# Kernel tuning notes

Measured on AMD Instinct MI355X. Metric: run time of the kernel, lower is better.

Reference implementation:

```python
import jax, jax.numpy as jnp
import numpy as np

B, L, D = 32, 2048, 1024


def setup_inputs() -> dict:
    key = jax.random.key(0)
    ks = jax.random.split(key, 8)
    s = 1.0 / np.sqrt(D).astype(np.float32)  # torch nn.Linear init scale
    return {
        "decoder_hidden": jax.random.normal(ks[0], (B, 1, D), jnp.float32),
        "encoder_outputs": jax.random.normal(ks[1], (B, L, D), jnp.float32),
        "W_w": jax.random.uniform(ks[2], (D, D), jnp.float32, -s, s),
        "W_b": jax.random.uniform(ks[3], (D,), jnp.float32, -s, s),
        "U_w": jax.random.uniform(ks[4], (D, D), jnp.float32, -s, s),
        "U_b": jax.random.uniform(ks[5], (D,), jnp.float32, -s, s),
        "v_w": jax.random.uniform(ks[6], (1, D), jnp.float32, -s, s),
        "v_b": jax.random.uniform(ks[7], (1,), jnp.float32, -s, s),
    }


def reference(decoder_hidden, encoder_outputs, W_w, W_b, U_w, U_b, v_w, v_b):
    # torch Linear: y = x @ W.T + b
    q = decoder_hidden @ W_w.T + W_b            # [B, 1, D]
    k = encoder_outputs @ U_w.T + U_b           # [B, L, D]
    scores = jnp.tanh(q + k) @ v_w.T + v_b      # [B, L, 1]
    attn = jax.nn.softmax(scores[..., 0], axis=-1)[:, None, :]  # [B, 1, L]
    context = jnp.einsum("bql,bld->bqd", attn, encoder_outputs)  # [B, 1, D]
    return (context, attn)
```

## Files before the change

kernel.cpp:

```cpp
#include <hip/hip_runtime.h>
#include <hip/hip_bf16.h>
#include <stdint.h>

#define BB 32
#define LL 2048
#define DD 1024

typedef short short8  __attribute__((ext_vector_type(8)));
typedef float f32x4   __attribute__((ext_vector_type(4)));

__device__ __forceinline__ short f2bf(float f) {
    unsigned u = __float_as_uint(f);
    u += 0x7fffu + ((u >> 16) & 1u);
    return (short)(u >> 16);
}

__device__ __forceinline__ float bf2f(unsigned short s) {
    return __uint_as_float(((unsigned)s) << 16);
}

__device__ __forceinline__ float fast_tanh(float x) {
    float e = __expf(2.f * x);
    return 1.f - 2.f * __builtin_amdgcn_rcpf(e + 1.f);
}

__device__ __forceinline__ void async_cp16(const void* g, void* l) {
    __builtin_amdgcn_global_load_lds(
        (__attribute__((address_space(1))) void*)g,
        (__attribute__((address_space(3))) void*)l, 16, 0, 0);
}

__global__ void cvt_bf16_kernel(const float* __restrict__ src, short* __restrict__ dst) {
    int idx = (blockIdx.x * 256 + threadIdx.x) * 8;
    float4 a = *(const float4*)(src + idx);
    float4 c = *(const float4*)(src + idx + 4);
    short8 p;
    p[0] = f2bf(a.x); p[1] = f2bf(a.y); p[2] = f2bf(a.z); p[3] = f2bf(a.w);
    p[4] = f2bf(c.x); p[5] = f2bf(c.y); p[6] = f2bf(c.z); p[7] = f2bf(c.w);
    *(short8*)(dst + idx) = p;
}

__global__ void q_kernel(const float* __restrict__ dh, const float* __restrict__ Ww,
                         const float* __restrict__ Wb, const float* __restrict__ Ub,
                         float* __restrict__ qbuf) {
    int b  = blockIdx.x >> 4;
    int d0 = (blockIdx.x & 15) << 6;
    int t = threadIdx.x, w = t >> 6, lane = t & 63;
    __shared__ __align__(16) float hs[DD];
    *(float4*)&hs[t * 4] = *(const float4*)&dh[b * DD + t * 4];
    __syncthreads();
    float hr[16];
#pragma unroll
    for (int i = 0; i < 16; i++) hr[i] = hs[lane + 64 * i];
    for (int i = 0; i < 16; i++) {
        int d = d0 + w * 16 + i;
        const float* wr = Ww + (size_t)d * DD;
        float s = 0.f;
#pragma unroll
        for (int j = 0; j < 16; j++) s += wr[lane + 64 * j] * hr[j];
#pragma unroll
        for (int m = 1; m < 64; m <<= 1) s += __shfl_xor(s, m, 64);
        if (lane == 0) qbuf[b * DD + d] = s + Wb[d] + Ub[d];
    }
}

__global__ __launch_bounds__(256, 3) void gemm_scores_bf(
    const short* __restrict__ encbf, const short* __restrict__ Ubf,
    const float* __restrict__ qbuf, const float* __restrict__ vw,
    float* __restrict__ spart) {
    __shared__ __align__(16) short As[128 * 32];
    __shared__ __align__(16) short Bs[128 * 32];
    __shared__ float q_s[128], v_s[128], s_acc[2][128];

    const int t = threadIdx.x;
    const int lane = t & 63, w = t >> 6;
    const int l15 = lane & 15, quad = lane >> 4;
    const int wm = w >> 1, wn = w & 1;

    const int lin  = blockIdx.x + (blockIdx.y << 3);
    const int xcd  = lin & 7;
    const int slot = lin >> 3;
    const int nblk = slot & 7;
    const int mstripe = (xcd << 6) + (slot >> 3);
    const int n0 = nblk << 7;
    const int m0 = mstripe << 7;
    const int b  = m0 >> 11;

    if (t < 128) {
        q_s[t] = qbuf[(b << 10) + n0 + t];
        v_s[t] = vw[n0 + t];
    }

    f32x4 acc[4][4];
#pragma unroll
    for (int i = 0; i < 4; i++)
#pragma unroll
        for (int j = 0; j < 4; j++) acc[i][j] = (f32x4){0.f, 0.f, 0.f, 0.f};

    const int srow = lane >> 2, sseg = (lane & 3) << 3;
    const short* gA0 = encbf + (((size_t)(m0 + w * 32 + srow)) << 10) + sseg;
    const short* gB0 = Ubf   + (((size_t)(n0 + w * 32 + srow)) << 10) + sseg;
    short* lA0 = As + w * 32 * 32;
    short* lB0 = Bs + w * 32 * 32;

    for (int k0 = 0; k0 < 1024; k0 += 32) {
        __syncthreads();
        async_cp16(gA0 + k0, lA0);
        async_cp16(gA0 + k0 + (16 << 10), lA0 + 16 * 32);
        async_cp16(gB0 + k0, lB0);
        async_cp16(gB0 + k0 + (16 << 10), lB0 + 16 * 32);
        __syncthreads();

        short8 af[4], bfv[4];
#pragma unroll
        for (int mt = 0; mt < 4; mt++)
            af[mt] = *(const short8*)&As[(wm * 64 + mt * 16 + l15) * 32 + quad * 8];
#pragma unroll
        for (int nt = 0; nt < 4; nt++)
            bfv[nt] = *(const short8*)&Bs[(wn * 64 + nt * 16 + l15) * 32 + quad * 8];
#pragma unroll
        for (int mt = 0; mt < 4; mt++)
#pragma unroll
            for (int nt = 0; nt < 4; nt++)
                acc[mt][nt] = __builtin_amdgcn_mfma_f32_16x16x32_bf16(
                    af[mt], bfv[nt], acc[mt][nt], 0, 0, 0);
    }

    float qn[4], vn[4];
#pragma unroll
    for (int nt = 0; nt < 4; nt++) {
        qn[nt] = q_s[wn * 64 + nt * 16 + l15];
        vn[nt] = v_s[wn * 64 + nt * 16 + l15];
    }
#pragma unroll
    for (int mt = 0; mt < 4; mt++) {
#pragma unroll
        for (int r = 0; r < 4; r++) {
            float sum = 0.f;
#pragma unroll
            for (int nt = 0; nt < 4; nt++)
                sum += vn[nt] * fast_tanh(acc[mt][nt][r] + qn[nt]);
            sum += __shfl_xor(sum, 1, 64);
            sum += __shfl_xor(sum, 2, 64);
            sum += __shfl_xor(sum, 4, 64);
            sum += __shfl_xor(sum, 8, 64);
            if (l15 == 0)
                s_acc[wn][wm * 64 + mt * 16 + quad * 4 + r] = sum;
        }
    }
    __syncthreads();
    if (t < 128)
        spart[((size_t)nblk << 16) + m0 + t] = s_acc[0][t] + s_acc[1][t];
}

__global__ void ctx_softmax_bf(const float* __restrict__ sp, const short* __restrict__ encbf,
                               float* __restrict__ attn, float* __restrict__ ctx) {
    const int dchunk = blockIdx.x, b = blockIdx.y;
    const int t = threadIdx.x;
    const int w = t >> 6, lane = t & 63;
    __shared__ float at_s[2048];
    __shared__ float red[16][128];
    __shared__ float rr[8];

    float v[4];
#pragma unroll
    for (int i = 0; i < 4; i++) {
        int l = t + (i << 9);
        float s = 0.f;
#pragma unroll
        for (int p = 0; p < 8; p++) s += sp[(p << 16) + (b << 11) + l];
        v[i] = s;
    }
    float m = fmaxf(fmaxf(v[0], v[1]), fmaxf(v[2], v[3]));
#pragma unroll
    for (int s = 1; s < 64; s <<= 1) m = fmaxf(m, __shfl_xor(m, s, 64));
    if (lane == 0) rr[w] = m;
    __syncthreads();
    m = rr[0];
#pragma unroll
    for (int i = 1; i < 8; i++) m = fmaxf(m, rr[i]);
    float s = 0.f;
#pragma unroll
    for (int i = 0; i < 4; i++) { v[i] = __expf(v[i] - m); s += v[i]; }
#pragma unroll
    for (int k = 1; k < 64; k <<= 1) s += __shfl_xor(s, k, 64);
    __syncthreads();
    if (lane == 0) rr[w] = s;
#pragma unroll
    for (int i = 0; i < 4; i++) at_s[t + (i << 9)] = v[i];
    __syncthreads();
    s = 0.f;
#pragma unroll
    for (int i = 0; i < 8; i++) s += rr[i];
    float inv = 1.f / s;

    if (dchunk == 0) {
#pragma unroll
        for (int i = 0; i < 4; i++) attn[(b << 11) + t + (i << 9)] = v[i] * inv;
    }

    const int d4 = (t & 31) << 2;
    const int dl = t >> 5;
    const int d0 = dchunk << 7;
    const short* base = encbf + ((size_t)b << 21) + d0 + d4;
    float ax = 0.f, ay = 0.f, az = 0.f, aw = 0.f;
#pragma unroll 4
    for (int i = 0; i < 128; i++) {
        int l = (i << 4) + dl;
        float wg = at_s[l];
        ushort4 e = *(const ushort4*)(base + ((size_t)l << 10));
        ax += wg * bf2f(e.x); ay += wg * bf2f(e.y);
        az += wg * bf2f(e.z); aw += wg * bf2f(e.w);
    }
    red[dl][d4 + 0] = ax;
    red[dl][d4 + 1] = ay;
    red[dl][d4 + 2] = az;
    red[dl][d4 + 3] = aw;
    __syncthreads();
    if (t < 128) {
        float acc = 0.f;
#pragma unroll
        for (int j = 0; j < 16; j++) acc += red[j][t];
        ctx[(b << 10) + d0 + t] = acc * inv;
    }
}

__global__ __launch_bounds__(256, 3) void gemm_scores_f32(
    const float* __restrict__ enc, const short* __restrict__ Ubf,
    const float* __restrict__ qbuf, const float* __restrict__ vw,
    float* __restrict__ scores) {
    __shared__ __align__(16) short As[128 * 32];
    __shared__ __align__(16) short Bs[128 * 32];
    __shared__ float q_s[128], v_s[128], s_acc[128];

    const int t = threadIdx.x;
    const int lane = t & 63, w = t >> 6;
    const int l15 = lane & 15, quad = lane >> 4;
    const int wm = w >> 1, wn = w & 1;
    const int n0 = blockIdx.x << 7;
    const int m0 = blockIdx.y << 7;
    const int b  = m0 >> 11;

    if (t < 128) {
        q_s[t] = qbuf[(b << 10) + n0 + t];
        v_s[t] = vw[n0 + t];
        s_acc[t] = 0.f;
    }

    f32x4 acc[4][4];
#pragma unroll
    for (int i = 0; i < 4; i++)
#pragma unroll
        for (int j = 0; j < 4; j++) acc[i][j] = (f32x4){0.f, 0.f, 0.f, 0.f};

    const int arow = t >> 1, ahalf = t & 1;
    const float* aptr = enc + (((size_t)(m0 + arow)) << 10) + (ahalf << 4);
    short* adst = As + arow * 32 + ahalf * 16;
    const int brow = t >> 2, bks = (t & 3) * 8;
    const short* bptr1 = Ubf + ((size_t)(n0 + brow)) * 1024 + bks;
    const short* bptr2 = bptr1 + (size_t)64 * 1024;
    short* bdst1 = Bs + brow * 32 + bks;
    short* bdst2 = bdst1 + 64 * 32;

    for (int k0 = 0; k0 < 1024; k0 += 32) {
        __syncthreads();
        float4 f0 = *(const float4*)(aptr + k0);
        float4 f1 = *(const float4*)(aptr + k0 + 4);
        float4 f2 = *(const float4*)(aptr + k0 + 8);
        float4 f3 = *(const float4*)(aptr + k0 + 12);
        short8 p0, p1;
        p0[0] = f2bf(f0.x); p0[1] = f2bf(f0.y); p0[2] = f2bf(f0.z); p0[3] = f2bf(f0.w);
        p0[4] = f2bf(f1.x); p0[5] = f2bf(f1.y); p0[6] = f2bf(f1.z); p0[7] = f2bf(f1.w);
        p1[0] = f2bf(f2.x); p1[1] = f2bf(f2.y); p1[2] = f2bf(f2.z); p1[3] = f2bf(f2.w);
        p1[4] = f2bf(f3.x); p1[5] = f2bf(f3.y); p1[6] = f2bf(f3.z); p1[7] = f2bf(f3.w);
        *(short8*)adst = p0;
        *(short8*)(adst + 8) = p1;
        *(short8*)bdst1 = *(const short8*)(bptr1 + k0);
        *(short8*)bdst2 = *(const short8*)(bptr2 + k0);
        __syncthreads();

        short8 af[4], bfv[4];
#pragma unroll
        for (int mt = 0; mt < 4; mt++)
            af[mt] = *(const short8*)&As[(wm * 64 + mt * 16 + l15) * 32 + quad * 8];
#pragma unroll
        for (int nt = 0; nt < 4; nt++)
            bfv[nt] = *(const short8*)&Bs[(wn * 64 + nt * 16 + l15) * 32 + quad * 8];
#pragma unroll
        for (int mt = 0; mt < 4; mt++)
#pragma unroll
            for (int nt = 0; nt < 4; nt++)
                acc[mt][nt] = __builtin_amdgcn_mfma_f32_16x16x32_bf16(
                    af[mt], bfv[nt], acc[mt][nt], 0, 0, 0);
    }

    float qn[4], vn[4];
#pragma unroll
    for (int nt = 0; nt < 4; nt++) {
        qn[nt] = q_s[wn * 64 + nt * 16 + l15];
        vn[nt] = v_s[wn * 64 + nt * 16 + l15];
    }
#pragma unroll
    for (int mt = 0; mt < 4; mt++) {
#pragma unroll
        for (int r = 0; r < 4; r++) {
            float sum = 0.f;
#pragma unroll
            for (int nt = 0; nt < 4; nt++)
                sum += vn[nt] * fast_tanh(acc[mt][nt][r] + qn[nt]);
            sum += __shfl_xor(sum, 1, 64);
            sum += __shfl_xor(sum, 2, 64);
            sum += __shfl_xor(sum, 4, 64);
            sum += __shfl_xor(sum, 8, 64);
            if (l15 == 0)
                atomicAdd(&s_acc[wm * 64 + mt * 16 + quad * 4 + r], sum);
        }
    }
    __syncthreads();
    if (t < 128) atomicAdd(&scores[m0 + t], s_acc[t]);
}

__global__ void softmax_kernel(const float* __restrict__ sp, float* __restrict__ attn) {
    int b = blockIdx.x, t = threadIdx.x;
    int w = t >> 6, lane = t & 63;
    __shared__ float rm[4], rs[4];
    float v[8];
#pragma unroll
    for (int i = 0; i < 8; i++) v[i] = sp[(b << 11) + t + (i << 8)];
    float m = v[0];
#pragma unroll
    for (int i = 1; i < 8; i++) m = fmaxf(m, v[i]);
#pragma unroll
    for (int s = 1; s < 64; s <<= 1) m = fmaxf(m, __shfl_xor(m, s, 64));
    if (lane == 0) rm[w] = m;
    __syncthreads();
    m = fmaxf(fmaxf(rm[0], rm[1]), fmaxf(rm[2], rm[3]));
    float s = 0.f;
#pragma unroll
    for (int i = 0; i < 8; i++) { v[i] = __expf(v[i] - m); s += v[i]; }
#pragma unroll
    for (int k = 1; k < 64; k <<= 1) s += __shfl_xor(s, k, 64);
    if (lane == 0) rs[w] = s;
    __syncthreads();
    s = rs[0] + rs[1] + rs[2] + rs[3];
    float inv = 1.f / s;
#pragma unroll
    for (int i = 0; i < 8; i++) attn[(b << 11) + t + (i << 8)] = v[i] * inv;
}

__global__ void context_f32(const float* __restrict__ enc, const float* __restrict__ attn,
                            float* __restrict__ ctx) {
    int dchunk = blockIdx.x, b = blockIdx.y;
    int t = threadIdx.x;
    __shared__ __align__(16) float at_s[2048];
    __shared__ float red[16][128];
    *(float4*)&at_s[t * 4] = *(const float4*)&attn[(b << 11) + t * 4];
    __syncthreads();
    int d4 = (t & 31) << 2;
    int dl = t >> 5;
    int d0 = dchunk << 7;
    const float* base = enc + ((size_t)b << 21) + d0 + d4;
    float ax = 0.f, ay = 0.f, az = 0.f, aw = 0.f;
#pragma unroll 4
    for (int i = 0; i < 128; i++) {
        int l = (i << 4) + dl;
        float wg = at_s[l];
        float4 e = *(const float4*)(base + ((size_t)l << 10));
        ax += wg * e.x; ay += wg * e.y; az += wg * e.z; aw += wg * e.w;
    }
    red[dl][d4 + 0] = ax;
    red[dl][d4 + 1] = ay;
    red[dl][d4 + 2] = az;
    red[dl][d4 + 3] = aw;
    __syncthreads();
    if (t < 128) {
        float s = 0.f;
#pragma unroll
        for (int j = 0; j < 16; j++) s += red[j][t];
        ctx[(b << 10) + d0 + t] = s;
    }
}

extern "C" void kernel_launch(void* const* d_in, const int* in_sizes, int n_in,
                              void* d_out, int out_size, void* d_ws, size_t ws_size,
                              hipStream_t stream) {
    const float* dh  = (const float*)d_in[0];
    const float* enc = (const float*)d_in[1];
    const float* Ww  = (const float*)d_in[2];
    const float* Wb  = (const float*)d_in[3];
    const float* Uw  = (const float*)d_in[4];
    const float* Ub  = (const float*)d_in[5];
    const float* vw  = (const float*)d_in[6];

    float* out  = (float*)d_out;
    float* attn = out + BB * DD;
    char*  ws   = (char*)d_ws;
    short* Ubf   = (short*)ws;
    float* qbuf  = (float*)(ws + (2 << 20));
    float* sbuf  = (float*)(ws + (2 << 20) + (1 << 17));
    short* encbf = (short*)(ws + (8 << 20));

    bool bigws = ws_size >= ((size_t)143 << 20);

    cvt_bf16_kernel<<<512, 256, 0, stream>>>(Uw, Ubf);
    q_kernel<<<512, 256, 0, stream>>>(dh, Ww, Wb, Ub, qbuf);

    if (bigws) {
        cvt_bf16_kernel<<<32768, 256, 0, stream>>>(enc, encbf);
        gemm_scores_bf<<<dim3(8, 512), 256, 0, stream>>>(encbf, Ubf, qbuf, vw, sbuf);
        ctx_softmax_bf<<<dim3(8, BB), 512, 0, stream>>>(sbuf, encbf, attn, out);
    } else {
        hipMemsetAsync(sbuf, 0, (size_t)BB * LL * sizeof(float), stream);
        gemm_scores_f32<<<dim3(8, 512), 256, 0, stream>>>(enc, Ubf, qbuf, vw, sbuf);
        softmax_kernel<<<BB, 256, 0, stream>>>(sbuf, attn);
        context_f32<<<dim3(8, BB), 512, 0, stream>>>(enc, attn, out);
    }
}
```

Measured before the change: 592.9 us.

## Fuse prep kernels into one launch and stage K=64 per barrier in bf16 GEMM

```diff
diff --git a/kernel.cpp b/kernel.cpp
--- a/kernel.cpp
+++ b/kernel.cpp
@@ -30,22 +30,28 @@
         (__attribute__((address_space(3))) void*)l, 16, 0, 0);
 }
 
-__global__ void cvt_bf16_kernel(const float* __restrict__ src, short* __restrict__ dst) {
-    int idx = (blockIdx.x * 256 + threadIdx.x) * 8;
-    float4 a = *(const float4*)(src + idx);
-    float4 c = *(const float4*)(src + idx + 4);
-    short8 p;
-    p[0] = f2bf(a.x); p[1] = f2bf(a.y); p[2] = f2bf(a.z); p[3] = f2bf(a.w);
-    p[4] = f2bf(c.x); p[5] = f2bf(c.y); p[6] = f2bf(c.z); p[7] = f2bf(c.w);
-    *(short8*)(dst + idx) = p;
-}
-
-__global__ void q_kernel(const float* __restrict__ dh, const float* __restrict__ Ww,
-                         const float* __restrict__ Wb, const float* __restrict__ Ub,
-                         float* __restrict__ qbuf) {
-    int b  = blockIdx.x >> 4;
-    int d0 = (blockIdx.x & 15) << 6;
-    int t = threadIdx.x, w = t >> 6, lane = t & 63;
+__global__ void prep_kernel(const float* __restrict__ dh, const float* __restrict__ Ww,
+                            const float* __restrict__ Wb, const float* __restrict__ Ub,
+                            const float* __restrict__ Uw, const float* __restrict__ enc,
+                            float* __restrict__ qbuf, short* __restrict__ Ubf,
+                            short* __restrict__ encbf) {
+    const int bid = blockIdx.x, t = threadIdx.x;
+    if (bid >= 512) {
+        const float* src = (bid < 1024) ? Uw : enc;
+        short* dst = (bid < 1024) ? Ubf : encbf;
+        int base = (bid < 1024) ? (bid - 512) : (bid - 1024);
+        size_t idx = ((size_t)base * 256 + t) * 8;
+        float4 a = *(const float4*)(src + idx);
+        float4 c = *(const float4*)(src + idx + 4);
+        short8 p;
+        p[0] = f2bf(a.x); p[1] = f2bf(a.y); p[2] = f2bf(a.z); p[3] = f2bf(a.w);
+        p[4] = f2bf(c.x); p[5] = f2bf(c.y); p[6] = f2bf(c.z); p[7] = f2bf(c.w);
+        *(short8*)(dst + idx) = p;
+        return;
+    }
+    int b  = bid >> 4;
+    int d0 = (bid & 15) << 6;
+    int w = t >> 6, lane = t & 63;
     __shared__ __align__(16) float hs[DD];
     *(float4*)&hs[t * 4] = *(const float4*)&dh[b * DD + t * 4];
     __syncthreads();
@@ -68,8 +74,8 @@
     const short* __restrict__ encbf, const short* __restrict__ Ubf,
     const float* __restrict__ qbuf, const float* __restrict__ vw,
     float* __restrict__ spart) {
-    __shared__ __align__(16) short As[128 * 32];
-    __shared__ __align__(16) short Bs[128 * 32];
+    __shared__ __align__(16) short As[2][128 * 32];
+    __shared__ __align__(16) short Bs[2][128 * 32];
     __shared__ float q_s[128], v_s[128], s_acc[2][128];
 
     const int t = threadIdx.x;
@@ -100,30 +106,36 @@
     const int srow = lane >> 2, sseg = (lane & 3) << 3;
     const short* gA0 = encbf + (((size_t)(m0 + w * 32 + srow)) << 10) + sseg;
     const short* gB0 = Ubf   + (((size_t)(n0 + w * 32 + srow)) << 10) + sseg;
-    short* lA0 = As + w * 32 * 32;
-    short* lB0 = Bs + w * 32 * 32;
-
-    for (int k0 = 0; k0 < 1024; k0 += 32) {
+    const int lofs = w * 32 * 32;
+
+    for (int k0 = 0; k0 < 1024; k0 += 64) {
         __syncthreads();
-        async_cp16(gA0 + k0, lA0);
-        async_cp16(gA0 + k0 + (16 << 10), lA0 + 16 * 32);
-        async_cp16(gB0 + k0, lB0);
-        async_cp16(gB0 + k0 + (16 << 10), lB0 + 16 * 32);
+        async_cp16(gA0 + k0,                 &As[0][lofs]);
+        async_cp16(gA0 + k0 + (16 << 10),    &As[0][lofs + 16 * 32]);
+        async_cp16(gB0 + k0,                 &Bs[0][lofs]);
+        async_cp16(gB0 + k0 + (16 << 10),    &Bs[0][lofs + 16 * 32]);
+        async_cp16(gA0 + k0 + 32,            &As[1][lofs]);
+        async_cp16(gA0 + k0 + 32 + (16 << 10), &As[1][lofs + 16 * 32]);
+        async_cp16(gB0 + k0 + 32,            &Bs[1][lofs]);
+        async_cp16(gB0 + k0 + 32 + (16 << 10), &Bs[1][lofs + 16 * 32]);
         __syncthreads();
 
-        short8 af[4], bfv[4];
-#pragma unroll
-        for (int mt = 0; mt < 4; mt++)
-            af[mt] = *(const short8*)&As[(wm * 64 + mt * 16 + l15) * 32 + quad * 8];
-#pragma unroll
-        for (int nt = 0; nt < 4; nt++)
-            bfv[nt] = *(const short8*)&Bs[(wn * 64 + nt * 16 + l15) * 32 + quad * 8];
-#pragma unroll
-        for (int mt = 0; mt < 4; mt++)
+#pragma unroll
+        for (int h = 0; h < 2; h++) {
+            short8 af[4], bfv[4];
+#pragma unroll
+            for (int mt = 0; mt < 4; mt++)
+                af[mt] = *(const short8*)&As[h][(wm * 64 + mt * 16 + l15) * 32 + quad * 8];
 #pragma unroll
             for (int nt = 0; nt < 4; nt++)
-                acc[mt][nt] = __builtin_amdgcn_mfma_f32_16x16x32_bf16(
-                    af[mt], bfv[nt], acc[mt][nt], 0, 0, 0);
+                bfv[nt] = *(const short8*)&Bs[h][(wn * 64 + nt * 16 + l15) * 32 + quad * 8];
+#pragma unroll
+            for (int mt = 0; mt < 4; mt++)
+#pragma unroll
+                for (int nt = 0; nt < 4; nt++)
+                    acc[mt][nt] = __builtin_amdgcn_mfma_f32_16x16x32_bf16(
+                        af[mt], bfv[nt], acc[mt][nt], 0, 0, 0);
+        }
     }
 
     float qn[4], vn[4];
@@ -222,6 +234,40 @@
 #pragma unroll
         for (int j = 0; j < 16; j++) acc += red[j][t];
         ctx[(b << 10) + d0 + t] = acc * inv;
+    }
+}
+
+__global__ void cvt_bf16_kernel(const float* __restrict__ src, short* __restrict__ dst) {
+    int idx = (blockIdx.x * 256 + threadIdx.x) * 8;
+    float4 a = *(const float4*)(src + idx);
+    float4 c = *(const float4*)(src + idx + 4);
+    short8 p;
+    p[0] = f2bf(a.x); p[1] = f2bf(a.y); p[2] = f2bf(a.z); p[3] = f2bf(a.w);
+    p[4] = f2bf(c.x); p[5] = f2bf(c.y); p[6] = f2bf(c.z); p[7] = f2bf(c.w);
+    *(short8*)(dst + idx) = p;
+}
+
+__global__ void q_kernel(const float* __restrict__ dh, const float* __restrict__ Ww,
+                         const float* __restrict__ Wb, const float* __restrict__ Ub,
+                         float* __restrict__ qbuf) {
+    int b  = blockIdx.x >> 4;
+    int d0 = (blockIdx.x & 15) << 6;
+    int t = threadIdx.x, w = t >> 6, lane = t & 63;
+    __shared__ __align__(16) float hs[DD];
+    *(float4*)&hs[t * 4] = *(const float4*)&dh[b * DD + t * 4];
+    __syncthreads();
+    float hr[16];
+#pragma unroll
+    for (int i = 0; i < 16; i++) hr[i] = hs[lane + 64 * i];
+    for (int i = 0; i < 16; i++) {
+        int d = d0 + w * 16 + i;
+        const float* wr = Ww + (size_t)d * DD;
+        float s = 0.f;
+#pragma unroll
+        for (int j = 0; j < 16; j++) s += wr[lane + 64 * j] * hr[j];
+#pragma unroll
+        for (int m = 1; m < 64; m <<= 1) s += __shfl_xor(s, m, 64);
+        if (lane == 0) qbuf[b * DD + d] = s + Wb[d] + Ub[d];
     }
 }
 
@@ -402,15 +448,14 @@
 
     bool bigws = ws_size >= ((size_t)143 << 20);
 
-    cvt_bf16_kernel<<<512, 256, 0, stream>>>(Uw, Ubf);
-    q_kernel<<<512, 256, 0, stream>>>(dh, Ww, Wb, Ub, qbuf);
-
     if (bigws) {
-        cvt_bf16_kernel<<<32768, 256, 0, stream>>>(enc, encbf);
+        prep_kernel<<<33792, 256, 0, stream>>>(dh, Ww, Wb, Ub, Uw, enc, qbuf, Ubf, encbf);
         gemm_scores_bf<<<dim3(8, 512), 256, 0, stream>>>(encbf, Ubf, qbuf, vw, sbuf);
         ctx_softmax_bf<<<dim3(8, BB), 512, 0, stream>>>(sbuf, encbf, attn, out);
     } else {
         hipMemsetAsync(sbuf, 0, (size_t)BB * LL * sizeof(float), stream);
+        cvt_bf16_kernel<<<512, 256, 0, stream>>>(Uw, Ubf);
+        q_kernel<<<512, 256, 0, stream>>>(dh, Ww, Wb, Ub, qbuf);
         gemm_scores_f32<<<dim3(8, 512), 256, 0, stream>>>(enc, Ubf, qbuf, vw, sbuf);
         softmax_kernel<<<BB, 256, 0, stream>>>(sbuf, attn);
         context_f32<<<dim3(8, BB), 512, 0, stream>>>(enc, attn, out);
```

After: 559.3 us. 5.7% less time.
